# Kernel optimization log

Measured on AMD Instinct MI355X. Metric: run time of the kernel, lower is better.

The kernel has to match this reference:

```python
import jax, jax.numpy as jnp
import numpy as np

D_MODEL = 1024
N_HEADS = 16
D_K = D_MODEL // N_HEADS
B, S = 2, 2048
NEG = -1.0e9


def setup_inputs() -> dict:
    key = jax.random.key(0)
    ks = jax.random.split(key, 12)
    sc = 1.0 / np.sqrt(D_MODEL)
    inp = {
        'query': jax.random.normal(ks[0], (B, S, D_MODEL), jnp.float32),
        'key': jax.random.normal(ks[1], (B, S, D_MODEL), jnp.float32),
        'value': jax.random.normal(ks[2], (B, S, D_MODEL), jnp.float32),
        # causal mask, broadcast over batch: 1 = attend, 0 = masked
        'mask': jnp.broadcast_to(jnp.tril(jnp.ones((S, S), jnp.int32)), (B, S, S)),
        'wq': jax.random.normal(ks[3], (D_MODEL, D_MODEL), jnp.float32) * sc,
        'bq': jnp.zeros((D_MODEL,), jnp.float32),
        'wk': jax.random.normal(ks[4], (D_MODEL, D_MODEL), jnp.float32) * sc,
        'bk': jnp.zeros((D_MODEL,), jnp.float32),
        'wv': jax.random.normal(ks[5], (D_MODEL, D_MODEL), jnp.float32) * sc,
        'bv': jnp.zeros((D_MODEL,), jnp.float32),
        'wo': jax.random.normal(ks[6], (D_MODEL, D_MODEL), jnp.float32) * sc,
        'bo': jnp.zeros((D_MODEL,), jnp.float32),
    }
    return inp


def reference(query, key, value, mask, wq, bq, wk, bk, wv, bv, wo, bo):
    b, sq, _ = query.shape
    sk = key.shape[1]
    # linear projections, split into heads: [B, H, S, d_k]
    def proj(x, w, bias, s):
        return (x @ w + bias).reshape(b, s, N_HEADS, D_K).transpose(0, 2, 1, 3)
    Q = proj(query, wq, bq, sq)
    K = proj(key, wk, bk, sk)
    V = proj(value, wv, bv, sk)
    # scaled dot-product attention with full score matrix [B, H, Sq, Sk]
    scores = jnp.einsum('bhqd,bhkd->bhqk', Q, K) / np.sqrt(D_K)
    scores = jnp.where(mask[:, None, :, :] == 0, NEG, scores)
    attn = jax.nn.softmax(scores, axis=-1)
    ctx = jnp.einsum('bhqk,bhkd->bhqd', attn, V)
    ctx = ctx.transpose(0, 2, 1, 3).reshape(b, sq, D_MODEL)
    return ctx @ wo + bo
```

## Files before the change

kernel.cpp:

```cpp
#include <hip/hip_runtime.h>
#include <stdint.h>

#define AS1 __attribute__((address_space(1)))
#define AS3 __attribute__((address_space(3)))

typedef __attribute__((ext_vector_type(8))) __bf16 bf16x8;
typedef __attribute__((ext_vector_type(4))) float f32x4;
typedef __attribute__((ext_vector_type(4))) unsigned int u32x4;
typedef __attribute__((ext_vector_type(2))) unsigned int u32x2;

static __device__ __forceinline__ void gload16(const void* g, void* l) {
    __builtin_amdgcn_global_load_lds((AS1 void*)(uintptr_t)g, (AS3 void*)l, 16, 0, 0);
}

static __device__ __forceinline__ unsigned cvt_pk_bf16(float lo, float hi) {
    unsigned r;
    asm volatile("v_cvt_pk_bf16_f32 %0, %1, %2" : "=v"(r) : "v"(lo), "v"(hi));
    return r;
}
static __device__ __forceinline__ unsigned short f2bf(float f) {
    return (unsigned short)(cvt_pk_bf16(f, 0.f) & 0xffffu);
}

static __device__ __forceinline__ f32x4 mfma16(bf16x8 a, bf16x8 b, f32x4 c) {
    return __builtin_amdgcn_mfma_f32_16x16x32_bf16(a, b, c, 0, 0, 0);
}

__global__ __launch_bounds__(256) void k_wtrans4(const float* __restrict__ w0,
                                                 const float* __restrict__ w1,
                                                 const float* __restrict__ w2,
                                                 const float* __restrict__ w3,
                                                 unsigned short* __restrict__ o0,
                                                 unsigned short* __restrict__ o1,
                                                 unsigned short* __restrict__ o2,
                                                 unsigned short* __restrict__ o3) {
    const float* W;
    unsigned short* Wt;
    switch (blockIdx.z) {
        case 0: W = w0; Wt = o0; break;
        case 1: W = w1; Wt = o1; break;
        case 2: W = w2; Wt = o2; break;
        default: W = w3; Wt = o3; break;
    }
    __shared__ unsigned short tile[64][72];
    const int tid = threadIdx.x;
    const int k0 = blockIdx.x * 64, n0 = blockIdx.y * 64;
#pragma unroll
    for (int j = 0; j < 4; ++j) {
        int c = j * 256 + tid;
        int kr = c >> 4, c4 = c & 15;
        f32x4 v = *(const f32x4*)(W + (size_t)(k0 + kr) * 1024 + n0 + c4 * 4);
#pragma unroll
        for (int e = 0; e < 4; ++e) tile[c4 * 4 + e][kr] = f2bf(v[e]);
    }
    __syncthreads();
#pragma unroll
    for (int j = 0; j < 2; ++j) {
        int c = j * 256 + tid;
        int nr = c >> 3, kc = c & 7;
        union { unsigned short s[8]; u32x4 v; } t;
#pragma unroll
        for (int e = 0; e < 8; ++e) t.s[e] = tile[nr][kc * 8 + e];
        *(u32x4*)(Wt + (size_t)(n0 + nr) * 1024 + k0 + kc * 8) = t.v;
    }
}

__global__ __launch_bounds__(256, 3) void k_gemm_qkv(
    const float* __restrict__ q, const float* __restrict__ k, const float* __restrict__ v,
    const unsigned short* __restrict__ Wq, const unsigned short* __restrict__ Wk,
    const unsigned short* __restrict__ Wv,
    const float* __restrict__ bq, const float* __restrict__ bk, const float* __restrict__ bv,
    unsigned short* __restrict__ Q2, unsigned short* __restrict__ K2,
    unsigned short* __restrict__ V2) {
    __shared__ __align__(16) char smem[32768];
    char* sA = smem;
    char* sB = smem + 16384;

    const float* A; const unsigned short* Bt; const float* bias; unsigned short* C; float sc;
    switch (blockIdx.z) {
        case 0:  A = q; Bt = Wq; bias = bq; C = Q2; sc = 0.18033688011112042f; break;
        case 1:  A = k; Bt = Wk; bias = bk; C = K2; sc = 1.0f; break;
        default: A = v; Bt = Wv; bias = bv; C = V2; sc = 1.0f; break;
    }
    const int tid = threadIdx.x;
    const int wave = tid >> 6, lane = tid & 63, g = lane >> 4, l16 = lane & 15;
    const int wm = wave & 1, wn = wave >> 1;
    const int m0 = blockIdx.x * 128, n0 = blockIdx.y * 128;
    const int K = 1024, N = 1024;

    const int arow = tid >> 1, ahalf = tid & 1;
    const float* asrc = A + (size_t)(m0 + arow) * K + ahalf * 32;

    f32x4 acc[4][4];
#pragma unroll
    for (int i = 0; i < 4; ++i)
#pragma unroll
        for (int j = 0; j < 4; ++j) acc[i][j] = (f32x4){0.f, 0.f, 0.f, 0.f};

    f32x4 ar[8];
#pragma unroll
    for (int i = 0; i < 8; ++i) ar[i] = *(const f32x4*)(asrc + i * 4);

    const int nkt = K >> 6;
#pragma unroll 1
    for (int kt = 0; kt < nkt; ++kt) {
        const int k0 = kt << 6;
        __syncthreads();
#pragma unroll
        for (int j = 0; j < 4; ++j) {
            int c = j * 256 + tid;
            int row = c >> 3, wch = c & 7, kc = wch ^ (row & 7);
            gload16(Bt + (size_t)(n0 + row) * K + k0 + kc * 8, sB + c * 16);
        }
        unsigned aw[16];
#pragma unroll
        for (int i = 0; i < 8; ++i) {
            aw[2 * i]     = cvt_pk_bf16(ar[i][0], ar[i][1]);
            aw[2 * i + 1] = cvt_pk_bf16(ar[i][2], ar[i][3]);
        }
#pragma unroll
        for (int j = 0; j < 4; ++j) {
            u32x4 wv = {aw[4 * j], aw[4 * j + 1], aw[4 * j + 2], aw[4 * j + 3]};
            int cw = ahalf * 4 + j;
            *(u32x4*)(sA + arow * 128 + ((cw ^ (arow & 7)) << 4)) = wv;
        }
        if (kt + 1 < nkt) {
#pragma unroll
            for (int i = 0; i < 8; ++i)
                ar[i] = *(const f32x4*)(asrc + ((kt + 1) << 6) + i * 4);
        }
        __syncthreads();
#pragma unroll
        for (int ks = 0; ks < 2; ++ks) {
            bf16x8 af[4], bfr[4];
#pragma unroll
            for (int mi = 0; mi < 4; ++mi) {
                int row = wm * 64 + mi * 16 + l16;
                int c = (ks * 4 + g) ^ (row & 7);
                af[mi] = *(const bf16x8*)(sA + row * 128 + c * 16);
            }
#pragma unroll
            for (int ni = 0; ni < 4; ++ni) {
                int row = wn * 64 + ni * 16 + l16;
                int c = (ks * 4 + g) ^ (row & 7);
                bfr[ni] = *(const bf16x8*)(sB + row * 128 + c * 16);
            }
#pragma unroll
            for (int mi = 0; mi < 4; ++mi)
#pragma unroll
                for (int ni = 0; ni < 4; ++ni)
                    acc[mi][ni] = mfma16(af[mi], bfr[ni], acc[mi][ni]);
        }
    }
#pragma unroll
    for (int ni = 0; ni < 4; ++ni) {
        int col = n0 + wn * 64 + ni * 16 + l16;
        float bn = bias[col];
#pragma unroll
        for (int mi = 0; mi < 4; ++mi) {
            int rbase = m0 + wm * 64 + mi * 16 + g * 4;
#pragma unroll
            for (int r = 0; r < 4; ++r)
                C[(size_t)(rbase + r) * N + col] = f2bf((acc[mi][ni][r] + bn) * sc);
        }
    }
}

template <int A_F32, int OUT_F32>
static __device__ __forceinline__ void gemm_body(const void* __restrict__ Ap,
                                                 const unsigned short* __restrict__ Bt,
                                                 const float* __restrict__ bias,
                                                 void* __restrict__ Cp,
                                                 int M, int N, int K, float cscale,
                                                 char* smem) {
    constexpr int ASZ = A_F32 ? 16384 : 8192;
    char* sA = smem;
    char* sB = smem + 2 * ASZ;
    const int tid = threadIdx.x;
    const int wave = tid >> 6, lane = tid & 63, g = lane >> 4, l16 = lane & 15;
    const int wm = wave & 1, wn = wave >> 1;
    const int m0 = blockIdx.x * 64, n0 = blockIdx.y * 128;

    f32x4 acc[2][4];
#pragma unroll
    for (int i = 0; i < 2; ++i)
#pragma unroll
        for (int j = 0; j < 4; ++j) acc[i][j] = (f32x4){0.f, 0.f, 0.f, 0.f};

    auto STAGE = [&](int k0, int buf) {
        if constexpr (A_F32) {
            const float* A = (const float*)Ap;
            char* dst = sA + buf * ASZ;
#pragma unroll
            for (int j = 0; j < 4; ++j) {
                int c = j * 256 + tid;
                int row = c >> 4, w = c & 15, kc = w ^ (row & 15);
                gload16(A + (size_t)(m0 + row) * K + k0 + kc * 4, dst + c * 16);
            }
        } else {
            const unsigned short* A = (const unsigned short*)Ap;
            char* dst = sA + buf * ASZ;
#pragma unroll
            for (int j = 0; j < 2; ++j) {
                int c = j * 256 + tid;
                int row = c >> 3, w = c & 7, kc = w ^ (row & 7);
                gload16(A + (size_t)(m0 + row) * K + k0 + kc * 8, dst + c * 16);
            }
        }
        char* dst = sB + buf * 16384;
#pragma unroll
        for (int j = 0; j < 4; ++j) {
            int c = j * 256 + tid;
            int row = c >> 3, w = c & 7, kc = w ^ (row & 7);
            gload16(Bt + (size_t)(n0 + row) * K + k0 + kc * 8, dst + c * 16);
        }
    };

    const int nkt = K >> 6;
    STAGE(0, 0);
    __syncthreads();
    int cur = 0;
#pragma unroll 1
    for (int kt = 0; kt < nkt; ++kt) {
        if (kt + 1 < nkt) STAGE((kt + 1) << 6, cur ^ 1);
        const char* sAc = sA + cur * ASZ;
        const char* sBc = sB + cur * 16384;
#pragma unroll
        for (int ks = 0; ks < 2; ++ks) {
            bf16x8 af[2];
#pragma unroll
            for (int mi = 0; mi < 2; ++mi) {
                int row = wm * 32 + mi * 16 + l16;
                if constexpr (A_F32) {
                    int c0 = (ks * 8 + g * 2) ^ (row & 15);
                    int c1 = (ks * 8 + g * 2 + 1) ^ (row & 15);
                    f32x4 lo = *(const f32x4*)(sAc + row * 256 + c0 * 16);
                    f32x4 hi = *(const f32x4*)(sAc + row * 256 + c1 * 16);
                    union { unsigned u[4]; bf16x8 v; } cv;
                    cv.u[0] = cvt_pk_bf16(lo[0], lo[1]);
                    cv.u[1] = cvt_pk_bf16(lo[2], lo[3]);
                    cv.u[2] = cvt_pk_bf16(hi[0], hi[1]);
                    cv.u[3] = cvt_pk_bf16(hi[2], hi[3]);
                    af[mi] = cv.v;
                } else {
                    int c = (ks * 4 + g) ^ (row & 7);
                    af[mi] = *(const bf16x8*)(sAc + row * 128 + c * 16);
                }
            }
#pragma unroll
            for (int ni = 0; ni < 4; ++ni) {
                int row = wn * 64 + ni * 16 + l16;
                int c = (ks * 4 + g) ^ (row & 7);
                bf16x8 bfr = *(const bf16x8*)(sBc + row * 128 + c * 16);
#pragma unroll
                for (int mi = 0; mi < 2; ++mi)
                    acc[mi][ni] = mfma16(af[mi], bfr, acc[mi][ni]);
            }
        }
        __syncthreads();
        cur ^= 1;
    }
#pragma unroll
    for (int ni = 0; ni < 4; ++ni) {
        int col = n0 + wn * 64 + ni * 16 + l16;
        float bn = bias[col];
#pragma unroll
        for (int mi = 0; mi < 2; ++mi) {
            int rbase = m0 + wm * 32 + mi * 16 + g * 4;
#pragma unroll
            for (int r = 0; r < 4; ++r) {
                float v = (acc[mi][ni][r] + bn) * cscale;
                if constexpr (OUT_F32)
                    ((float*)Cp)[(size_t)(rbase + r) * N + col] = v;
                else
                    ((unsigned short*)Cp)[(size_t)(rbase + r) * N + col] = f2bf(v);
            }
        }
    }
}

__global__ __launch_bounds__(256) void k_gemm_o(const unsigned short* __restrict__ ctx,
                                                const unsigned short* __restrict__ Wo,
                                                const float* __restrict__ bo,
                                                float* __restrict__ out) {
    extern __shared__ __align__(16) char smem[];
    gemm_body<0, 1>(ctx, Wo, bo, out, 4096, 1024, 1024, 1.0f, smem);
}

__global__ __launch_bounds__(256) void k_vtrans(const unsigned short* __restrict__ V2,
                                                unsigned short* __restrict__ Vt) {
    __shared__ unsigned short tile[64][72];
    const int tid = threadIdx.x;
    const int s0 = blockIdx.x * 64;
    const int bh = blockIdx.y, b = bh >> 4, h = bh & 15;
#pragma unroll
    for (int j = 0; j < 2; ++j) {
        int c = j * 256 + tid;
        int sr = c >> 3, dc = c & 7;
        union { u32x4 v; unsigned short s[8]; } t;
        t.v = *(const u32x4*)(V2 + (size_t)(b * 2048 + s0 + sr) * 1024 + h * 64 + dc * 8);
#pragma unroll
        for (int e = 0; e < 8; ++e) tile[dc * 8 + e][sr] = t.s[e];
    }
    __syncthreads();
#pragma unroll
    for (int j = 0; j < 2; ++j) {
        int c = j * 256 + tid;
        int dr = c >> 3, sc = c & 7;
        union { unsigned short s[8]; u32x4 v; } t;
#pragma unroll
        for (int e = 0; e < 8; ++e) t.s[e] = tile[dr][sc * 8 + e];
        *(u32x4*)(Vt + ((size_t)bh * 64 + dr) * 2048 + s0 + sc * 8) = t.v;
    }
}

__global__ __launch_bounds__(128) void k_attn(const unsigned short* __restrict__ Q2,
                                              const unsigned short* __restrict__ K2,
                                              const unsigned short* __restrict__ Vt,
                                              unsigned short* __restrict__ ctx) {
    __shared__ __align__(16) char sK[8192];
    __shared__ __align__(16) char sV[2][8192];
    __shared__ __align__(16) char sP[2][2048];

    const int tid = threadIdx.x, w = tid >> 6, lane = tid & 63;
    const int g = lane >> 4, l16 = lane & 15;
    const int bid = blockIdx.x;
    const int xcd = bid & 7, j = bid >> 3;
    const int bh = xcd * 4 + (j & 3);
    const int t = 63 - (j >> 2);
    const int b = bh >> 4, h = bh & 15;
    const int swzl = (l16 & 7) << 4;

    const int r0 = tid >> 3;
    const int sc0 = (tid & 7) ^ (r0 & 7);
    const unsigned short* ksrc = K2 + (size_t)(b * 2048 + r0) * 1024 + h * 64 + sc0 * 8;
    const unsigned short* vsrc = Vt + ((size_t)bh * 64 + r0) * 2048 + sc0 * 8;
    char* const myp = sP[w];

    const int wq0 = t * 32 + w * 16;
    const int qg = wq0 + l16;

    const unsigned short* qp = Q2 + (size_t)(b * 2048 + wq0 + l16) * 1024 + h * 64;
    bf16x8 qf0 = *(const bf16x8*)(qp + g * 8);
    bf16x8 qf1 = *(const bf16x8*)(qp + 32 + g * 8);

    f32x4 accO[4];
#pragma unroll
    for (int i = 0; i < 4; ++i) accO[i] = (f32x4){0.f, 0.f, 0.f, 0.f};
    float m = 0.f, lsum = 0.f;

    const int nkv = (t >> 1) + 1;
    const int diag = t >> 1;
#pragma unroll
    for (int rr = 0; rr < 4; ++rr) {
        gload16(ksrc + (size_t)(rr * 16) * 1024, sK + rr * 2048 + tid * 16);
        gload16(vsrc + (size_t)(rr * 16) * 2048, sV[0] + rr * 2048 + tid * 16);
    }
    __syncthreads();

#pragma unroll 1
    for (int kt = 0; kt < nkv; ++kt) {
        const int cur = kt & 1;
        const int kv0 = kt * 64;
        float s[16];
        __builtin_amdgcn_s_setprio(1);
#pragma unroll
        for (int blk = 0; blk < 4; ++blk) {
            const int rl = blk * 16 + l16;
            const char* krow = sK + rl * 128;
            bf16x8 kf0 = *(const bf16x8*)(krow + ((g << 4) ^ swzl));
            bf16x8 kf1 = *(const bf16x8*)(krow + (((4 + g) << 4) ^ swzl));
            f32x4 a = (f32x4){0.f, 0.f, 0.f, 0.f};
            a = mfma16(kf0, qf0, a);
            a = mfma16(kf1, qf1, a);
#pragma unroll
            for (int rr = 0; rr < 4; ++rr) s[blk * 4 + rr] = a[rr];
        }
        __builtin_amdgcn_s_setprio(0);
        __syncthreads();
        if (kt + 1 < nkv) {
#pragma unroll
            for (int rr = 0; rr < 4; ++rr) {
                gload16(ksrc + (size_t)(kv0 + 64 + rr * 16) * 1024, sK + rr * 2048 + tid * 16);
                gload16(vsrc + (size_t)(rr * 16) * 2048 + (kv0 + 64), sV[cur ^ 1] + rr * 2048 + tid * 16);
            }
        }
        if (kt == diag) {
#pragma unroll
            for (int j2 = 0; j2 < 16; ++j2) {
                int kvg = kv0 + (j2 >> 2) * 16 + g * 4 + (j2 & 3);
                if (kvg > qg) s[j2] = -1e9f;
            }
        }
        float ps = 0.f;
        unsigned pk[8];
#pragma unroll
        for (int j2 = 0; j2 < 8; ++j2) {
            float p0 = __builtin_exp2f(s[2 * j2] - m);
            float p1 = __builtin_exp2f(s[2 * j2 + 1] - m);
            ps += p0 + p1;
            pk[j2] = cvt_pk_bf16(p0, p1);
        }
        if (__any(ps > 16777216.f)) {
            float c1 = fmaxf(fmaxf(s[0], s[1]), s[2]);
            c1 = fmaxf(fmaxf(c1, s[3]), s[4]);
            c1 = fmaxf(fmaxf(c1, s[5]), s[6]);
            c1 = fmaxf(c1, s[7]);
            float c2 = fmaxf(fmaxf(s[8], s[9]), s[10]);
            c2 = fmaxf(fmaxf(c2, s[11]), s[12]);
            c2 = fmaxf(fmaxf(c2, s[13]), s[14]);
            c2 = fmaxf(c2, s[15]);
            float mx = fmaxf(c1, c2);
            mx = fmaxf(mx, __shfl_xor(mx, 16));
            mx = fmaxf(mx, __shfl_xor(mx, 32));
            float mnew = fmaxf(m, mx);
            float scl = __builtin_exp2f(m - mnew);
            lsum *= scl;
#pragma unroll
            for (int dt = 0; dt < 4; ++dt) accO[dt] = accO[dt] * scl;
            m = mnew;
            ps = 0.f;
#pragma unroll
            for (int j2 = 0; j2 < 8; ++j2) {
                float p0 = __builtin_exp2f(s[2 * j2] - m);
                float p1 = __builtin_exp2f(s[2 * j2 + 1] - m);
                ps += p0 + p1;
                pk[j2] = cvt_pk_bf16(p0, p1);
            }
        }
        lsum += ps;
#pragma unroll
        for (int blk = 0; blk < 4; ++blk) {
            u32x2 pw = {pk[blk * 2], pk[blk * 2 + 1]};
            *(u32x2*)(myp + l16 * 128 + ((blk * 32 + g * 8) ^ swzl)) = pw;
        }
        __builtin_amdgcn_s_setprio(1);
#pragma unroll
        for (int kvh = 0; kvh < 2; ++kvh) {
            bf16x8 pf = *(const bf16x8*)(myp + l16 * 128 + ((kvh * 64 + g * 16) ^ swzl));
#pragma unroll
            for (int dt = 0; dt < 4; ++dt) {
                const int rv = dt * 16 + l16;
                bf16x8 vf = *(const bf16x8*)(sV[cur] + rv * 128 + (((kvh * 4 + g) << 4) ^ swzl));
                accO[dt] = mfma16(vf, pf, accO[dt]);
            }
        }
        __builtin_amdgcn_s_setprio(0);
        __syncthreads();
    }
    float v = lsum;
    v += __shfl_xor(v, 16);
    v += __shfl_xor(v, 32);
    float inv = 1.f / v;
    unsigned short* cp = ctx + (size_t)(b * 2048 + wq0 + l16) * 1024 + h * 64 + g * 4;
#pragma unroll
    for (int dt = 0; dt < 4; ++dt) {
        u32x2 o;
        o[0] = cvt_pk_bf16(accO[dt][0] * inv, accO[dt][1] * inv);
        o[1] = cvt_pk_bf16(accO[dt][2] * inv, accO[dt][3] * inv);
        *(u32x2*)(cp + dt * 16) = o;
    }
}

extern "C" void kernel_launch(void* const* d_in, const int* in_sizes, int n_in,
                              void* d_out, int out_size, void* d_ws, size_t ws_size,
                              hipStream_t stream) {
    const float* query = (const float*)d_in[0];
    const float* key   = (const float*)d_in[1];
    const float* value = (const float*)d_in[2];
    const float* wq = (const float*)d_in[4];
    const float* bq = (const float*)d_in[5];
    const float* wk = (const float*)d_in[6];
    const float* bk = (const float*)d_in[7];
    const float* wv = (const float*)d_in[8];
    const float* bv = (const float*)d_in[9];
    const float* wo = (const float*)d_in[10];
    const float* bo = (const float*)d_in[11];
    float* out = (float*)d_out;

    char* ws = (char*)d_ws;
    unsigned short* Wtq = (unsigned short*)ws;
    unsigned short* Wtk = Wtq + 1024 * 1024;
    unsigned short* Wtv = Wtk + 1024 * 1024;
    unsigned short* Wto = Wtv + 1024 * 1024;
    unsigned short* Q2  = Wto + 1024 * 1024;
    unsigned short* K2  = Q2 + 4096 * 1024;
    unsigned short* V2  = K2 + 4096 * 1024;
    unsigned short* Vt  = V2 + 4096 * 1024;
    unsigned short* ctx = Vt + 4096 * 1024;

    dim3 blk(256);
    k_wtrans4<<<dim3(16, 16, 4), blk, 0, stream>>>(wq, wk, wv, wo, Wtq, Wtk, Wtv, Wto);

    k_gemm_qkv<<<dim3(32, 8, 3), blk, 0, stream>>>(query, key, value,
                                                   Wtq, Wtk, Wtv, bq, bk, bv,
                                                   Q2, K2, V2);

    k_vtrans<<<dim3(32, 32), blk, 0, stream>>>(V2, Vt);
    k_attn<<<dim3(2048), dim3(128), 0, stream>>>(Q2, K2, Vt, ctx);

    k_gemm_o<<<dim3(64, 8), blk, 49152, stream>>>(ctx, Wto, bo, out);
}
```

Baseline: 134.0 us.

## Double-buffer weight tiles in QKV GEMM and prefetch next stage before MFMA

The QKV projection GEMM now keeps two LDS buffers for the bf16 weight tile and issues the async global-to-LDS load for tile k+1 before running the MFMAs on tile k. The fp32 activation prefetch, bf16 conversion and LDS write are moved after the compute, and the MFMA section runs at raised wave priority via s_setprio. The aim is to hide global load latency behind matrix math. LDS use grows from 32 KB to 48 KB per block, which may limit the 3-blocks-per-CU occupancy target, and the loop still holds two barriers per iteration.

Result: slower. 140.1 us (+4.6%).

```diff
diff --git a/kernel.cpp b/kernel.cpp
--- a/kernel.cpp
+++ b/kernel.cpp
@@ -72,9 +72,8 @@
     const float* __restrict__ bq, const float* __restrict__ bk, const float* __restrict__ bv,
     unsigned short* __restrict__ Q2, unsigned short* __restrict__ K2,
     unsigned short* __restrict__ V2) {
-    __shared__ __align__(16) char smem[32768];
-    char* sA = smem;
-    char* sB = smem + 16384;
+    __shared__ __align__(16) char sA[16384];
+    __shared__ __align__(16) char sB[2][16384];
 
     const float* A; const unsigned short* Bt; const float* bias; unsigned short* C; float sc;
     switch (blockIdx.z) {
@@ -97,39 +96,50 @@
 #pragma unroll
         for (int j = 0; j < 4; ++j) acc[i][j] = (f32x4){0.f, 0.f, 0.f, 0.f};
 
-    f32x4 ar[8];
-#pragma unroll
-    for (int i = 0; i < 8; ++i) ar[i] = *(const f32x4*)(asrc + i * 4);
-
-    const int nkt = K >> 6;
-#pragma unroll 1
-    for (int kt = 0; kt < nkt; ++kt) {
-        const int k0 = kt << 6;
-        __syncthreads();
+    auto STAGE_B = [&](int k0, int buf) {
 #pragma unroll
         for (int j = 0; j < 4; ++j) {
             int c = j * 256 + tid;
             int row = c >> 3, wch = c & 7, kc = wch ^ (row & 7);
-            gload16(Bt + (size_t)(n0 + row) * K + k0 + kc * 8, sB + c * 16);
-        }
-        unsigned aw[16];
-#pragma unroll
-        for (int i = 0; i < 8; ++i) {
-            aw[2 * i]     = cvt_pk_bf16(ar[i][0], ar[i][1]);
-            aw[2 * i + 1] = cvt_pk_bf16(ar[i][2], ar[i][3]);
-        }
+            gload16(Bt + (size_t)(n0 + row) * K + k0 + kc * 8, sB[buf] + c * 16);
+        }
+    };
+    auto WRITE_A = [&](const unsigned* aw) {
 #pragma unroll
         for (int j = 0; j < 4; ++j) {
             u32x4 wv = {aw[4 * j], aw[4 * j + 1], aw[4 * j + 2], aw[4 * j + 3]};
             int cw = ahalf * 4 + j;
             *(u32x4*)(sA + arow * 128 + ((cw ^ (arow & 7)) << 4)) = wv;
         }
-        if (kt + 1 < nkt) {
+    };
+
+    STAGE_B(0, 0);
+    f32x4 ar[8];
+#pragma unroll
+    for (int i = 0; i < 8; ++i) ar[i] = *(const f32x4*)(asrc + i * 4);
+    {
+        unsigned aw[16];
+#pragma unroll
+        for (int i = 0; i < 8; ++i) {
+            aw[2 * i]     = cvt_pk_bf16(ar[i][0], ar[i][1]);
+            aw[2 * i + 1] = cvt_pk_bf16(ar[i][2], ar[i][3]);
+        }
+        WRITE_A(aw);
+    }
+    __syncthreads();
+
+    const int nkt = K >> 6;
+#pragma unroll 1
+    for (int kt = 0; kt < nkt; ++kt) {
+        const int cur = kt & 1;
+        const bool more = (kt + 1 < nkt);
+        if (more) {
+            STAGE_B((kt + 1) << 6, cur ^ 1);
 #pragma unroll
             for (int i = 0; i < 8; ++i)
                 ar[i] = *(const f32x4*)(asrc + ((kt + 1) << 6) + i * 4);
         }
-        __syncthreads();
+        __builtin_amdgcn_s_setprio(1);
 #pragma unroll
         for (int ks = 0; ks < 2; ++ks) {
             bf16x8 af[4], bfr[4];
@@ -143,13 +153,27 @@
             for (int ni = 0; ni < 4; ++ni) {
                 int row = wn * 64 + ni * 16 + l16;
                 int c = (ks * 4 + g) ^ (row & 7);
-                bfr[ni] = *(const bf16x8*)(sB + row * 128 + c * 16);
+                bfr[ni] = *(const bf16x8*)(sB[cur] + row * 128 + c * 16);
             }
 #pragma unroll
             for (int mi = 0; mi < 4; ++mi)
 #pragma unroll
                 for (int ni = 0; ni < 4; ++ni)
                     acc[mi][ni] = mfma16(af[mi], bfr[ni], acc[mi][ni]);
+        }
+        __builtin_amdgcn_s_setprio(0);
+        unsigned aw[16];
+        if (more) {
+#pragma unroll
+            for (int i = 0; i < 8; ++i) {
+                aw[2 * i]     = cvt_pk_bf16(ar[i][0], ar[i][1]);
+                aw[2 * i + 1] = cvt_pk_bf16(ar[i][2], ar[i][3]);
+            }
+        }
+        __syncthreads();
+        if (more) {
+            WRITE_A(aw);
+            __syncthreads();
         }
     }
 #pragma unroll
```
